# Kernel tuning notes

Measured on AMD Instinct MI355X. Metric: run time of the kernel, lower is better.

Reference implementation:

```python
import jax, jax.numpy as jnp
import numpy as np

EMB = 1280
MD = 200
N = 20000
E = 200000
LN_EPS = 1e-5


def _layer_norm(x, g, b):
    mu = jnp.mean(x, axis=-1, keepdims=True)
    var = jnp.mean((x - mu) ** 2, axis=-1, keepdims=True)
    return (x - mu) * jax.lax.rsqrt(var + LN_EPS) * g + b


def _gat_conv(x, edge_index, edge_attr, W, We, a_src, a_dst, a_edge, bias, heads, C):
    """PyG GATConv (bias-free lin, edge_dim, add_self_loops with fill='mean')."""
    n = x.shape[0]
    src, dst = edge_index[0], edge_index[1]
    # self-loop edge_attr = mean of incoming edge_attr per dst node (0 if none)
    cnt = jax.ops.segment_sum(jnp.ones((edge_attr.shape[0],), x.dtype), dst, n)
    s = jax.ops.segment_sum(edge_attr, dst, n)
    loop_attr = jnp.where(cnt[:, None] > 0, s / jnp.maximum(cnt, 1.0)[:, None], 0.0)
    loop = jnp.arange(n)
    src = jnp.concatenate([src, loop])
    dst = jnp.concatenate([dst, loop])
    ea = jnp.concatenate([edge_attr, loop_attr], axis=0)
    h = (x @ W).reshape(n, heads, C)                      # [N,H,C]
    al_s = jnp.einsum('nhc,hc->nh', h, a_src)
    al_d = jnp.einsum('nhc,hc->nh', h, a_dst)
    eh = (ea @ We).reshape(-1, heads, C)                  # [E+N,H,C]
    al_e = jnp.einsum('ehc,hc->eh', eh, a_edge)
    alpha = jax.nn.leaky_relu(al_s[src] + al_d[dst] + al_e, 0.2)
    amax = jax.ops.segment_max(alpha, dst, n)
    amax = jnp.where(jnp.isfinite(amax), amax, 0.0)
    ex = jnp.exp(alpha - amax[dst])
    denom = jax.ops.segment_sum(ex, dst, n)
    w = ex / (denom[dst] + 1e-16)                         # segment softmax over dst
    out = jax.ops.segment_sum(h[src] * w[:, :, None], dst, n)
    return out.reshape(n, heads * C) + bias


def _forward(x, edge_index, edge_attr,
             ca_qw, ca_qb, ca_kw, ca_kb, ca_vw, ca_vb, ca_ow, ca_ob,
             g0_w, g0_ew, g0_as, g0_ad, g0_ae, g0_b, ln0_g, ln0_b,
             g1_w, g1_ew, g1_as, g1_ad, g1_ae, g1_b, ln1_g, ln1_b,
             g2_w, g2_ew, g2_as, g2_ad, g2_ae, g2_b, ln2_g, ln2_b,
             cls_w1, cls_b1, cls_w2, cls_b2):
    xe = x[:, :EMB]
    md = x[0, EMB:]
    # CrossAttention: single md vector -> K,V are [1,hidden]
    Q = xe @ ca_qw + ca_qb                                # [N,hid]
    K = md @ ca_kw + ca_kb                                # [hid]
    V = md @ ca_vw + ca_vb                                # [hid]
    scores = (Q @ K) / jnp.sqrt(jnp.asarray(Q.shape[-1], Q.dtype))  # [N]
    wts = jax.nn.softmax(scores, axis=0)[:, None]         # softmax over nodes
    attended = wts * V[None, :]                           # [N,hid]
    h = attended @ ca_ow + ca_ob + xe                     # [N,EMB]

    h = _gat_conv(h, edge_index, edge_attr, g0_w, g0_ew, g0_as, g0_ad, g0_ae, g0_b, 4, 256)
    h = jax.nn.relu(_layer_norm(h, ln0_g, ln0_b))
    h = _gat_conv(h, edge_index, edge_attr, g1_w, g1_ew, g1_as, g1_ad, g1_ae, g1_b, 4, 256)
    h = jax.nn.relu(_layer_norm(h, ln1_g, ln1_b))
    h = _gat_conv(h, edge_index, edge_attr, g2_w, g2_ew, g2_as, g2_ad, g2_ae, g2_b, 1, 256)
    h = jax.nn.relu(_layer_norm(h, ln2_g, ln2_b))

    g = jnp.mean(h, axis=0, keepdims=True)                # [1,256]
    g = jax.nn.relu(g @ cls_w1 + cls_b1)
    return g @ cls_w2 + cls_b2                            # [1,2]


def setup_inputs() -> dict:
    key = jax.random.key(0)
    ks = jax.random.split(key, 64)
    i = [0]
    def nrm(shape, scale=0.05):
        i[0] += 1
        return jax.random.normal(ks[i[0]], shape, jnp.float32) * scale
    inp = {}
    inp['x'] = nrm((N, EMB + MD), 1.0)
    inp['edge_index'] = jax.random.randint(ks[60], (2, E), 0, N, jnp.int64 if jax.config.read('jax_enable_x64') else jnp.int32)
    inp['edge_attr'] = jax.random.uniform(ks[61], (E, 1), jnp.float32)
    inp.update(ca_qw=nrm((EMB, 256)), ca_qb=jnp.zeros((256,), jnp.float32),
               ca_kw=nrm((MD, 256)), ca_kb=jnp.zeros((256,), jnp.float32),
               ca_vw=nrm((MD, 256)), ca_vb=jnp.zeros((256,), jnp.float32),
               ca_ow=nrm((256, EMB)), ca_ob=jnp.zeros((EMB,), jnp.float32))
    inp.update(g0_w=nrm((EMB, 1024)), g0_ew=nrm((1, 1024)), g0_as=nrm((4, 256)),
               g0_ad=nrm((4, 256)), g0_ae=nrm((4, 256)), g0_b=jnp.zeros((1024,), jnp.float32),
               ln0_g=jnp.ones((1024,), jnp.float32), ln0_b=jnp.zeros((1024,), jnp.float32))
    inp.update(g1_w=nrm((1024, 1024)), g1_ew=nrm((1, 1024)), g1_as=nrm((4, 256)),
               g1_ad=nrm((4, 256)), g1_ae=nrm((4, 256)), g1_b=jnp.zeros((1024,), jnp.float32),
               ln1_g=jnp.ones((1024,), jnp.float32), ln1_b=jnp.zeros((1024,), jnp.float32))
    inp.update(g2_w=nrm((1024, 256)), g2_ew=nrm((1, 256)), g2_as=nrm((1, 256)),
               g2_ad=nrm((1, 256)), g2_ae=nrm((1, 256)), g2_b=jnp.zeros((256,), jnp.float32),
               ln2_g=jnp.ones((256,), jnp.float32), ln2_b=jnp.zeros((256,), jnp.float32))
    inp.update(cls_w1=nrm((256, 128)), cls_b1=jnp.zeros((128,), jnp.float32),
               cls_w2=nrm((128, 2)), cls_b2=jnp.zeros((2,), jnp.float32))
    return inp


def reference(x, edge_index, edge_attr,
              ca_qw, ca_qb, ca_kw, ca_kb, ca_vw, ca_vb, ca_ow, ca_ob,
              g0_w, g0_ew, g0_as, g0_ad, g0_ae, g0_b, ln0_g, ln0_b,
              g1_w, g1_ew, g1_as, g1_ad, g1_ae, g1_b, ln1_g, ln1_b,
              g2_w, g2_ew, g2_as, g2_ad, g2_ae, g2_b, ln2_g, ln2_b,
              cls_w1, cls_b1, cls_w2, cls_b2):
    return _forward(x, edge_index, edge_attr,
                    ca_qw, ca_qb, ca_kw, ca_kb, ca_vw, ca_vb, ca_ow, ca_ob,
                    g0_w, g0_ew, g0_as, g0_ad, g0_ae, g0_b, ln0_g, ln0_b,
                    g1_w, g1_ew, g1_as, g1_ad, g1_ae, g1_b, ln1_g, ln1_b,
                    g2_w, g2_ew, g2_as, g2_ad, g2_ae, g2_b, ln2_g, ln2_b,
                    cls_w1, cls_b1, cls_w2, cls_b2)
```

## Files before the change

kernel.cpp:

```cpp
#include <hip/hip_runtime.h>
#include <hip/hip_bf16.h>
#include <math.h>

#define N_NODES 20000
#define N_EDGES 200000
#define XROW    1480

typedef __attribute__((ext_vector_type(8))) _Float16 f16x8;
typedef __attribute__((ext_vector_type(8))) unsigned short u16x8;
typedef __attribute__((ext_vector_type(4))) float f32x4v;

__device__ __forceinline__ float wsum(float v){
#pragma unroll
  for (int o=32;o>0;o>>=1) v += __shfl_down(v,o);
  return v;
}
__device__ __forceinline__ float wmax(float v){
#pragma unroll
  for (int o=32;o>0;o>>=1) v = fmaxf(v,__shfl_down(v,o));
  return v;
}
__device__ __forceinline__ float wsum_all(float v){
#pragma unroll
  for (int o=32;o>0;o>>=1) v += __shfl_xor(v,o);
  return v;
}
__device__ __forceinline__ float wmax_all(float v){
#pragma unroll
  for (int o=32;o>0;o>>=1) v = fmaxf(v,__shfl_xor(v,o));
  return v;
}

__device__ __forceinline__ unsigned short f2hu(float f){
  _Float16 h = (_Float16)f;
  return __builtin_bit_cast(unsigned short, h);
}
__device__ __forceinline__ float hu2f(unsigned short u){
  return (float)__builtin_bit_cast(_Float16, u);
}

__device__ __forceinline__ void async_copy16(void* lds, const void* g){
  __builtin_amdgcn_global_load_lds((const __attribute__((address_space(1))) void*)g,
                                   (__attribute__((address_space(3))) void*)lds, 16, 0, 0);
}

__global__ void edge_count_kernel(const int* __restrict__ ei, const float* __restrict__ ea,
                                  int* __restrict__ cnt, float* __restrict__ easum, int E){
  int e = blockIdx.x*256 + threadIdx.x;
  if (e >= E) return;
  int dst = ei[E + e];
  atomicAdd(&cnt[dst], 1);
  atomicAdd(&easum[dst], ea[e]);
}

__launch_bounds__(1024)
__global__ void scan_kernel(const int* __restrict__ cnt, const float* __restrict__ easum,
                            int* __restrict__ off, float* __restrict__ loop_attr, int n){
  __shared__ int buf[1024];
  __shared__ int carry_s;
  if (threadIdx.x==0) carry_s = 0;
  __syncthreads();
  for (int base=0; base<n; base+=1024){
    int i = base + threadIdx.x;
    int v = (i<n)? cnt[i] : 0;
    if (i<n){
      loop_attr[i] = (v>0) ? easum[i]/(float)v : 0.f;
    }
    buf[threadIdx.x] = v;
    __syncthreads();
    for (int d2=1; d2<1024; d2<<=1){
      int tv = (threadIdx.x>=d2)? buf[threadIdx.x-d2] : 0;
      __syncthreads();
      buf[threadIdx.x] += tv;
      __syncthreads();
    }
    if (i<n) off[i] = carry_s + buf[threadIdx.x] - v;
    int tot = buf[1023];
    __syncthreads();
    if (threadIdx.x==0) carry_s += tot;
    __syncthreads();
  }
  if (threadIdx.x==0) off[n] = carry_s;
}

__global__ void edge_fill_kernel(const int* __restrict__ ei, const float* __restrict__ ea,
                                 const int* __restrict__ off, int* __restrict__ fill,
                                 int* __restrict__ csr_src, float* __restrict__ csr_ea, int E){
  int e = blockIdx.x*256 + threadIdx.x;
  if (e >= E) return;
  int dst = ei[E + e];
  int pos = off[dst] + atomicAdd(&fill[dst], 1);
  csr_src[pos] = ei[e];
  csr_ea[pos]  = ea[e];
}

__global__ void x_to_f16(const float* __restrict__ x, unsigned short* __restrict__ xh){
  const int CH4 = 1280/4;
  long total = (long)N_NODES*CH4;
  for (long i = (long)blockIdx.x*256 + threadIdx.x; i < total; i += (long)gridDim.x*256){
    int row = (int)(i / CH4), c4 = (int)(i % CH4);
    float4 v = *(const float4*)(x + (size_t)row*XROW + c4*4);
    ushort4 o;
    o.x = f2hu(v.x); o.y = f2hu(v.y); o.z = f2hu(v.z); o.w = f2hu(v.w);
    *(ushort4*)(xh + (size_t)row*1280 + c4*4) = o;
  }
}

__global__ void wt_f16_kernel(const float* __restrict__ W, int K, int N,
                              unsigned short* __restrict__ Wt){
  __shared__ float tile[32][33];
  int k0 = blockIdx.x*32, n0 = blockIdx.y*32;
  int tx = threadIdx.x & 31, ty = threadIdx.x >> 5;
  for (int r=ty; r<32; r+=8) tile[r][tx] = W[(size_t)(k0+r)*N + n0+tx];
  __syncthreads();
  for (int r=ty; r<32; r+=8){
    float w = tile[tx][r];
    Wt[(size_t)(n0+r)*K + k0+tx] = f2hu(w);
  }
}

__global__ void kv_kernel(const float* __restrict__ x,
                          const float* __restrict__ kw, const float* __restrict__ kb,
                          const float* __restrict__ vw, const float* __restrict__ vb,
                          float* __restrict__ Kv, float* __restrict__ Vv){
  int j = threadIdx.x;
  float ka = kb[j], va = vb[j];
  for (int k=0;k<200;k++){
    float m = x[1280+k];
    ka = fmaf(m, kw[k*256+j], ka);
    va = fmaf(m, vw[k*256+j], va);
  }
  Kv[j]=ka; Vv[j]=va;
}

__global__ void qkvo_kernel(const float* __restrict__ qw, const float* __restrict__ ow,
                            const float* __restrict__ Kv, const float* __restrict__ Vv,
                            float* __restrict__ qK, float* __restrict__ Vo){
  int idx = blockIdx.x*256 + threadIdx.x;
  if (idx < 1280){
    float a=0;
    for (int j=0;j<256;j++) a = fmaf(qw[idx*256+j], Kv[j], a);
    qK[idx]=a;
  } else if (idx < 2560){
    int j = idx-1280;
    float a=0;
    for (int i=0;i<256;i++) a = fmaf(Vv[i], ow[(size_t)i*1280+j], a);
    Vo[j]=a;
  }
}

__global__ void obw_kernel(const float* __restrict__ ob, const float* __restrict__ Vo,
                           const float* __restrict__ W, float* __restrict__ obW, float* __restrict__ VoW){
  int j = blockIdx.x*256 + threadIdx.x;
  float a=0,b=0;
  for (int i=0;i<1280;i++){
    float w = W[(size_t)i*1024+j];
    a = fmaf(ob[i], w, a);
    b = fmaf(Vo[i], w, b);
  }
  obW[j]=a; VoW[j]=b;
}

__launch_bounds__(256)
__global__ void scores_kernel(const float* __restrict__ x, const float* __restrict__ qK,
                              float* __restrict__ scores, int n){
  __shared__ float qs[1280];
  int t = threadIdx.x;
  for (int i=t;i<1280;i+=256) qs[i]=qK[i];
  __syncthreads();
  int wid = t>>6, lane = t&63;
  int node = blockIdx.x*4 + wid;
  if (node >= n) return;
  const float4* row = (const float4*)(x + (size_t)node*XROW);
  float acc = 0;
#pragma unroll
  for (int it=0; it<5; it++){
    float4 v = row[lane + 64*it];
    float4 q = *(const float4*)&qs[4*(lane+64*it)];
    acc += v.x*q.x + v.y*q.y + v.z*q.z + v.w*q.w;
  }
  acc = wsum(acc);
  if (lane==0) scores[node] = acc;
}

__launch_bounds__(1024)
__global__ void softmax_nodes(const float* __restrict__ scores, float* __restrict__ wts, int n){
  __shared__ float red[16];
  int t = threadIdx.x, lane=t&63, wid=t>>6;
  float m = -INFINITY;
  for (int i=t;i<n;i+=1024) m = fmaxf(m, scores[i]);
  m = wmax(m);
  if (lane==0) red[wid]=m;
  __syncthreads();
  if (t==0){ float r=red[0]; for (int k=1;k<16;k++) r=fmaxf(r,red[k]); red[0]=r; }
  __syncthreads();
  float M = red[0];
  __syncthreads();
  float z=0;
  for (int i=t;i<n;i+=1024) z += expf((scores[i]-M)*(1.f/16.f));
  z = wsum(z);
  if (lane==0) red[wid]=z;
  __syncthreads();
  if (t==0){ float r=0; for (int k=0;k<16;k++) r+=red[k]; red[0]=r; }
  __syncthreads();
  float invZ = 1.f/red[0];
  for (int i=t;i<n;i+=1024) wts[i] = expf((scores[i]-M)*(1.f/16.f))*invZ;
}

__launch_bounds__(256)
__global__ void gemm_f16(const unsigned short* __restrict__ A,
                         const unsigned short* __restrict__ B,
                         unsigned short* __restrict__ C, int M, int N, int K,
                         const float* __restrict__ addCol,
                         const float* __restrict__ vCol,
                         const float* __restrict__ wRow,
                         const float* __restrict__ a_src,
                         const float* __restrict__ a_dst,
                         float* __restrict__ als,
                         float* __restrict__ ald,
                         int H)
{
  __shared__ short lds[2*128*64];
  short* As = lds;
  short* Bs = lds + 128*64;

  const int ntc = N >> 7;
  const int sh  = __popc(ntc - 1);
  const int g   = blockIdx.y >> sh;
  const int nt  = blockIdx.y & (ntc - 1);
  const int band = blockIdx.x + (g << 3);
  if (band * 128 >= M) return;

  const int t = threadIdx.x;
  const int w = t>>6, l = t&63;
  const int bm = band*128, bn = nt*128;
  const int wr = (w>>1)*64, wc = (w&1)*64;

  f32x4v acc[4][4];
#pragma unroll
  for (int i=0;i<4;i++)
#pragma unroll
    for (int j=0;j<4;j++) acc[i][j] = (f32x4v){0.f,0.f,0.f,0.f};

  const unsigned short* Ap[4]; const unsigned short* Bp[4];
  int ldsOff[4];
#pragma unroll
  for (int q=0;q<4;q++){
    int p  = (w*4+q)*64 + l;
    int r  = p>>3, pc = p&7;
    int kc = (pc ^ (r&7))*8;
    int rowA = bm + r; if (rowA > M-1) rowA = M-1;
    Ap[q] = A + (size_t)rowA*K + kc;
    Bp[q] = B + (size_t)(bn+r)*K + kc;
    ldsOff[q] = (w*4+q)*64*8;
  }

  for (int k0=0; k0<K; k0+=64){
#pragma unroll
    for (int q=0;q<4;q++) async_copy16(As + ldsOff[q], Ap[q] + k0);
#pragma unroll
    for (int q=0;q<4;q++) async_copy16(Bs + ldsOff[q], Bp[q] + k0);
    __syncthreads();

    const int q4 = l>>4, m16 = l&15;
#pragma unroll
    for (int ks=0; ks<2; ks++){
      f16x8 af[4], bf[4];
      const int c = ks*4 + q4;
#pragma unroll
      for (int i=0;i<4;i++){
        int ra = wr + i*16 + m16;
        af[i] = *(const f16x8*)&As[ra*64 + ((c ^ (ra&7))*8)];
        int rb = wc + i*16 + m16;
        bf[i] = *(const f16x8*)&Bs[rb*64 + ((c ^ (rb&7))*8)];
      }
#pragma unroll
      for (int i=0;i<4;i++)
#pragma unroll
        for (int j=0;j<4;j++)
          acc[i][j] = __builtin_amdgcn_mfma_f32_16x16x32_f16(af[i], bf[j], acc[i][j], 0,0,0);
    }
    __syncthreads();
  }

  const int q4 = l>>4, m16 = l&15;
  const int hd = (bn + wc) >> 8;
  float asv[4], adv[4];
#pragma unroll
  for (int j=0;j<4;j++){
    int n = bn + wc + j*16 + m16;
    asv[j] = a_src[n];
    adv[j] = a_dst[n];
  }
#pragma unroll
  for (int i=0;i<4;i++){
#pragma unroll
    for (int r=0;r<4;r++){
      int m = bm + wr + i*16 + q4*4 + r;
      if (m >= M) continue;
      float wrow = addCol ? wRow[m] : 0.f;
      unsigned short* crow = C + (size_t)m*N;
      float vj[4];
#pragma unroll
      for (int j=0;j<4;j++){
        int n = bn + wc + j*16 + m16;
        float v = acc[i][j][r];
        if (addCol) v += addCol[n] + wrow*vCol[n];
        vj[j] = v;
        crow[n] = f2hu(v);
      }
      float s = vj[0]*asv[0] + vj[1]*asv[1] + vj[2]*asv[2] + vj[3]*asv[3];
      float d = vj[0]*adv[0] + vj[1]*adv[1] + vj[2]*adv[2] + vj[3]*adv[3];
#pragma unroll
      for (int o=1;o<16;o<<=1){ s += __shfl_xor(s,o); d += __shfl_xor(d,o); }
      if (m16 == 0){
        atomicAdd(&als[(size_t)m*H + hd], s);
        atomicAdd(&ald[(size_t)m*H + hd], d);
      }
    }
  }
}

template<int H>
__global__ void we_kernel(const float* __restrict__ We, const float* __restrict__ a_edge,
                          float* __restrict__ we){
  int wid = threadIdx.x>>6, lane = threadIdx.x&63;
  if (wid < H){
    const float4* w4 = (const float4*)(We + wid*256);
    const float4* a4 = (const float4*)(a_edge + wid*256);
    float4 a = w4[lane], b = a4[lane];
    float v = a.x*b.x + a.y*b.y + a.z*b.z + a.w*b.w;
    v = wsum(v);
    if (lane==0) we[wid]=v;
  }
}

template<int H>
__launch_bounds__(256)
__global__ void gat_agg_ln_wave(const unsigned short* __restrict__ hmat,
                           const float* __restrict__ als, const float* __restrict__ ald,
                           const int* __restrict__ off, const int* __restrict__ csr_src,
                           const float* __restrict__ csr_ea, const float* __restrict__ loop_attr,
                           const float* __restrict__ we,
                           const float* __restrict__ bias,
                           const float* __restrict__ ln_g, const float* __restrict__ ln_b,
                           float* __restrict__ outf, unsigned short* __restrict__ outb, int n)
{
  constexpr int OUT = 256*H;
  constexpr int CPL = OUT/64;
  const int wv = threadIdx.x>>6, lane = threadIdx.x&63;
  const int i = blockIdx.x*4 + wv;
  __shared__ float wbuf_s[4][64*H];
  __shared__ int   sbuf_s[4][64];
  if (i >= n) return;
  float* wbuf = wbuf_s[wv];
  int*   sbuf = sbuf_s[wv];

  const int begin = off[i];
  const int deg   = off[i+1]-begin;
  const int S     = deg + 1;

  float aldi[H], wei[H];
#pragma unroll
  for (int hh=0;hh<H;hh++){ aldi[hh]=ald[(size_t)i*H+hh]; wei[hh]=we[hh]; }
  const float lea = loop_attr[i];

  const int head = (lane*CPL) >> 8;
  const int c0   = lane*CPL;
  float acc[CPL];
#pragma unroll
  for (int c=0;c<CPL;c++) acc[c]=0.f;

  if (S <= 64){
    int src = i; float ev = lea;
    if (lane < deg){ src = csr_src[begin+lane]; ev = csr_ea[begin+lane]; }
    const bool act = lane < S;
    float a[H];
#pragma unroll
    for (int hh=0;hh<H;hh++){
      float v = als[(size_t)src*H+hh] + aldi[hh] + ev*wei[hh];
      a[hh] = v>0.f ? v : 0.2f*v;
    }
#pragma unroll
    for (int hh=0;hh<H;hh++){
      float M = wmax_all(act ? a[hh] : -INFINITY);
      float e = act ? __expf(a[hh]-M) : 0.f;
      float Z = wsum_all(e);
      wbuf[lane*H+hh] = e / (Z + 1e-16f);
    }
    sbuf[lane] = src;
    for (int j=0;j<S;j++){
      int sj = sbuf[j];
      float wj = wbuf[j*H+head];
      const unsigned short* row = hmat + (size_t)sj*OUT + c0;
      if constexpr (CPL==16){
        u16x8 r0 = *(const u16x8*)(row);
        u16x8 r1 = *(const u16x8*)(row+8);
#pragma unroll
        for (int c=0;c<8;c++){
          acc[c]   = fmaf(wj, hu2f(r0[c]), acc[c]);
          acc[8+c] = fmaf(wj, hu2f(r1[c]), acc[8+c]);
        }
      } else {
        ushort4 r = *(const ushort4*)(row);
        acc[0]=fmaf(wj,hu2f(r.x),acc[0]); acc[1]=fmaf(wj,hu2f(r.y),acc[1]);
        acc[2]=fmaf(wj,hu2f(r.z),acc[2]); acc[3]=fmaf(wj,hu2f(r.w),acc[3]);
      }
    }
  } else {
    float rm[H];
#pragma unroll
    for (int hh=0;hh<H;hh++) rm[hh] = -INFINITY;
    for (int s=lane; s<S; s+=64){
      int src = (s<deg)? csr_src[begin+s] : i;
      float ev = (s<deg)? csr_ea[begin+s] : lea;
#pragma unroll
      for (int hh=0;hh<H;hh++){
        float v = als[(size_t)src*H+hh] + aldi[hh] + ev*wei[hh];
        v = v>0.f? v : 0.2f*v;
        rm[hh] = fmaxf(rm[hh], v);
      }
    }
    float M[H], es[H];
#pragma unroll
    for (int hh=0;hh<H;hh++){ M[hh]=wmax_all(rm[hh]); es[hh]=0.f; }
    for (int s=lane; s<S; s+=64){
      int src = (s<deg)? csr_src[begin+s] : i;
      float ev = (s<deg)? csr_ea[begin+s] : lea;
#pragma unroll
      for (int hh=0;hh<H;hh++){
        float v = als[(size_t)src*H+hh] + aldi[hh] + ev*wei[hh];
        v = v>0.f? v : 0.2f*v;
        es[hh] += __expf(v - M[hh]);
      }
    }
    float invZ[H];
#pragma unroll
    for (int hh=0;hh<H;hh++) invZ[hh] = 1.f/(wsum_all(es[hh]) + 1e-16f);
    for (int cb=0; cb<S; cb+=64){
      int m = min(64, S-cb);
      int s = cb + lane;
      if (s < S){
        int src = (s<deg)? csr_src[begin+s] : i;
        float ev = (s<deg)? csr_ea[begin+s] : lea;
        sbuf[lane] = src;
#pragma unroll
        for (int hh=0;hh<H;hh++){
          float v = als[(size_t)src*H+hh] + aldi[hh] + ev*wei[hh];
          v = v>0.f? v : 0.2f*v;
          wbuf[lane*H+hh] = __expf(v - M[hh]) * invZ[hh];
        }
      }
      for (int j=0;j<m;j++){
        int sj = sbuf[j];
        float wj = wbuf[j*H+head];
        const unsigned short* row = hmat + (size_t)sj*OUT + c0;
        if constexpr (CPL==16){
          u16x8 r0 = *(const u16x8*)(row);
          u16x8 r1 = *(const u16x8*)(row+8);
#pragma unroll
          for (int c=0;c<8;c++){
            acc[c]   = fmaf(wj, hu2f(r0[c]), acc[c]);
            acc[8+c] = fmaf(wj, hu2f(r1[c]), acc[8+c]);
          }
        } else {
          ushort4 r = *(const ushort4*)(row);
          acc[0]=fmaf(wj,hu2f(r.x),acc[0]); acc[1]=fmaf(wj,hu2f(r.y),acc[1]);
          acc[2]=fmaf(wj,hu2f(r.z),acc[2]); acc[3]=fmaf(wj,hu2f(r.w),acc[3]);
        }
      }
    }
  }

  float vals[CPL];
  float ls=0.f;
#pragma unroll
  for (int c=0;c<CPL;c+=4){
    float4 b4 = *(const float4*)(bias + c0 + c);
    vals[c]=acc[c]+b4.x; vals[c+1]=acc[c+1]+b4.y; vals[c+2]=acc[c+2]+b4.z; vals[c+3]=acc[c+3]+b4.w;
    ls += vals[c]+vals[c+1]+vals[c+2]+vals[c+3];
  }
  float mu = wsum_all(ls) * (1.f/OUT);
  float lv=0.f;
#pragma unroll
  for (int c=0;c<CPL;c++){ float d=vals[c]-mu; lv += d*d; }
  float inv = rsqrtf(wsum_all(lv)*(1.f/OUT) + 1e-5f);

  if (outb){
#pragma unroll
    for (int c=0;c<CPL;c+=8){
      u16x8 o;
#pragma unroll
      for (int k=0;k<8;k++){
        float g = ln_g[c0+c+k], b = ln_b[c0+c+k];
        o[k] = f2hu(fmaxf((vals[c+k]-mu)*inv*g + b, 0.f));
      }
      *(u16x8*)(outb + (size_t)i*OUT + c0 + c) = o;
    }
    if constexpr (CPL==4){
    }
  }
  if (outb && CPL==4){
    ushort4 o;
    o.x = f2hu(fmaxf((vals[0]-mu)*inv*ln_g[c0+0] + ln_b[c0+0], 0.f));
    o.y = f2hu(fmaxf((vals[1]-mu)*inv*ln_g[c0+1] + ln_b[c0+1], 0.f));
    o.z = f2hu(fmaxf((vals[2]-mu)*inv*ln_g[c0+2] + ln_b[c0+2], 0.f));
    o.w = f2hu(fmaxf((vals[3]-mu)*inv*ln_g[c0+3] + ln_b[c0+3], 0.f));
    *(ushort4*)(outb + (size_t)i*OUT + c0) = o;
  }
  if (!outb){
#pragma unroll
    for (int c=0;c<CPL;c+=4){
      float4 g4 = *(const float4*)(ln_g + c0 + c);
      float4 b4 = *(const float4*)(ln_b + c0 + c);
      float4 o;
      o.x = fmaxf((vals[c+0]-mu)*inv*g4.x + b4.x, 0.f);
      o.y = fmaxf((vals[c+1]-mu)*inv*g4.y + b4.y, 0.f);
      o.z = fmaxf((vals[c+2]-mu)*inv*g4.z + b4.z, 0.f);
      o.w = fmaxf((vals[c+3]-mu)*inv*g4.w + b4.w, 0.f);
      *(float4*)(outf + (size_t)i*OUT + c0 + c) = o;
    }
  }
}

__global__ void colsum_kernel(const float* __restrict__ h2, float* __restrict__ gsum, int n){
  int c = threadIdx.x;
  float acc=0;
  for (int i=blockIdx.x;i<n;i+=gridDim.x) acc += h2[(size_t)i*256 + c];
  atomicAdd(&gsum[c], acc);
}

__launch_bounds__(128)
__global__ void cls_kernel(const float* __restrict__ gsum,
                           const float* __restrict__ w1, const float* __restrict__ b1,
                           const float* __restrict__ w2, const float* __restrict__ b2,
                           float* __restrict__ outp){
  __shared__ float g[256];
  __shared__ float hid[128];
  int t = threadIdx.x;
  g[t]     = gsum[t]    *(1.f/N_NODES);
  g[t+128] = gsum[t+128]*(1.f/N_NODES);
  __syncthreads();
  float a = b1[t];
  for (int c=0;c<256;c++) a = fmaf(g[c], w1[c*128+t], a);
  hid[t] = fmaxf(a, 0.f);
  __syncthreads();
  if (t<2){
    float o = b2[t];
    for (int j=0;j<128;j++) o = fmaf(hid[j], w2[j*2+t], o);
    outp[t] = o;
  }
}

extern "C" void kernel_launch(void* const* d_in, const int* in_sizes, int n_in,
                              void* d_out, int out_size, void* d_ws, size_t ws_size,
                              hipStream_t stream)
{
  const float* x      = (const float*)d_in[0];
  const int*   ei     = (const int*)  d_in[1];
  const float* ea     = (const float*)d_in[2];
  const float* ca_qw  = (const float*)d_in[3];
  const float* ca_kw  = (const float*)d_in[5];
  const float* ca_kb  = (const float*)d_in[6];
  const float* ca_vw  = (const float*)d_in[7];
  const float* ca_vb  = (const float*)d_in[8];
  const float* ca_ow  = (const float*)d_in[9];
  const float* ca_ob  = (const float*)d_in[10];
  const float* g0_w   = (const float*)d_in[11];
  const float* g0_ew  = (const float*)d_in[12];
  const float* g0_as  = (const float*)d_in[13];
  const float* g0_ad  = (const float*)d_in[14];
  const float* g0_ae  = (const float*)d_in[15];
  const float* g0_b   = (const float*)d_in[16];
  const float* ln0_g  = (const float*)d_in[17];
  const float* ln0_b  = (const float*)d_in[18];
  const float* g1_w   = (const float*)d_in[19];
  const float* g1_ew  = (const float*)d_in[20];
  const float* g1_as  = (const float*)d_in[21];
  const float* g1_ad  = (const float*)d_in[22];
  const float* g1_ae  = (const float*)d_in[23];
  const float* g1_b   = (const float*)d_in[24];
  const float* ln1_g  = (const float*)d_in[25];
  const float* ln1_b  = (const float*)d_in[26];
  const float* g2_w   = (const float*)d_in[27];
  const float* g2_ew  = (const float*)d_in[28];
  const float* g2_as  = (const float*)d_in[29];
  const float* g2_ad  = (const float*)d_in[30];
  const float* g2_ae  = (const float*)d_in[31];
  const float* g2_b   = (const float*)d_in[32];
  const float* ln2_g  = (const float*)d_in[33];
  const float* ln2_b  = (const float*)d_in[34];
  const float* cls_w1 = (const float*)d_in[35];
  const float* cls_b1 = (const float*)d_in[36];
  const float* cls_w2 = (const float*)d_in[37];
  const float* cls_b2 = (const float*)d_in[38];
  float* outp = (float*)d_out;

  const int N = N_NODES, E = N_EDGES;

  char* base = (char*)d_ws;
  size_t o = 0;
  auto alloc = [&](size_t bytes)->void*{
    void* p = base + o;
    o += (bytes + 255) & ~(size_t)255;
    return p;
  };
  unsigned short* hF   = (unsigned short*)alloc((size_t)N*1024*2);
  unsigned short* Af   = (unsigned short*)alloc((size_t)N*1280*2);
  float*          h2   = (float*)         alloc((size_t)N*256*4);
  unsigned short* Wt   = (unsigned short*)alloc((size_t)1280*1024*2);
  float* als       = (float*)alloc((size_t)2*N*4*4);
  float* ald       = als + (size_t)N*4;
  float* scores    = (float*)alloc((size_t)N*4);
  float* wts       = (float*)alloc((size_t)N*4);
  int*   cnt       = (int*)  alloc((size_t)N*4);
  float* easum     = (float*)alloc((size_t)N*4);
  int*   off       = (int*)  alloc((size_t)(N+1)*4);
  int*   fill      = (int*)  alloc((size_t)N*4);
  int*   csr_src   = (int*)  alloc((size_t)E*4);
  float* csr_ea    = (float*)alloc((size_t)E*4);
  float* loop_attr = (float*)alloc((size_t)N*4);
  float* Kv        = (float*)alloc(256*4);
  float* Vv        = (float*)alloc(256*4);
  float* qK        = (float*)alloc(1280*4);
  float* Vo        = (float*)alloc(1280*4);
  float* obW       = (float*)alloc(1024*4);
  float* VoW       = (float*)alloc(1024*4);
  float* web       = (float*)alloc(16*4);
  float* gsum      = (float*)alloc(256*4);

  hipMemsetAsync(cnt,   0, (size_t)N*4, stream);
  hipMemsetAsync(easum, 0, (size_t)N*4, stream);
  hipMemsetAsync(fill,  0, (size_t)N*4, stream);
  hipMemsetAsync(gsum,  0, 256*4,       stream);

  int eblocks = (E + 255)/256;
  edge_count_kernel<<<eblocks,256,0,stream>>>(ei, ea, cnt, easum, E);
  scan_kernel<<<1,1024,0,stream>>>(cnt, easum, off, loop_attr, N);
  edge_fill_kernel<<<eblocks,256,0,stream>>>(ei, ea, off, fill, csr_src, csr_ea, E);

  x_to_f16<<<2048,256,0,stream>>>(x, Af);

  kv_kernel<<<1,256,0,stream>>>(x, ca_kw, ca_kb, ca_vw, ca_vb, Kv, Vv);
  qkvo_kernel<<<10,256,0,stream>>>(ca_qw, ca_ow, Kv, Vv, qK, Vo);
  obw_kernel<<<4,256,0,stream>>>(ca_ob, Vo, g0_w, obW, VoW);
  scores_kernel<<<(N+3)/4,256,0,stream>>>(x, qK, scores, N);
  softmax_nodes<<<1,1024,0,stream>>>(scores, wts, N);

  const int mTiles  = (N + 127)/128;
  const int mGroups = (mTiles + 7)/8;
  const int NB4 = (N + 3)/4;

  wt_f16_kernel<<<dim3(1280/32, 1024/32),256,0,stream>>>(g0_w, 1280, 1024, Wt);
  hipMemsetAsync(als, 0, (size_t)2*N*4*4, stream);
  gemm_f16<<<dim3(8, mGroups*8),256,0,stream>>>(Af, Wt, hF, N, 1024, 1280, obW, VoW, wts,
                                                g0_as, g0_ad, als, ald, 4);
  we_kernel<4><<<1,256,0,stream>>>(g0_ew, g0_ae, web);
  gat_agg_ln_wave<4><<<NB4,256,0,stream>>>(hF, als, ald, off, csr_src, csr_ea, loop_attr,
                                           web, g0_b, ln0_g, ln0_b, nullptr, Af, N);

  wt_f16_kernel<<<dim3(1024/32, 1024/32),256,0,stream>>>(g1_w, 1024, 1024, Wt);
  hipMemsetAsync(als, 0, (size_t)2*N*4*4, stream);
  gemm_f16<<<dim3(8, mGroups*8),256,0,stream>>>(Af, Wt, hF, N, 1024, 1024, nullptr, nullptr, nullptr,
                                                g1_as, g1_ad, als, ald, 4);
  we_kernel<4><<<1,256,0,stream>>>(g1_ew, g1_ae, web);
  gat_agg_ln_wave<4><<<NB4,256,0,stream>>>(hF, als, ald, off, csr_src, csr_ea, loop_attr,
                                           web, g1_b, ln1_g, ln1_b, nullptr, Af, N);

  wt_f16_kernel<<<dim3(1024/32, 256/32),256,0,stream>>>(g2_w, 1024, 256, Wt);
  hipMemsetAsync(als, 0, (size_t)2*N*4*4, stream);
  gemm_f16<<<dim3(8, mGroups*2),256,0,stream>>>(Af, Wt, hF, N, 256, 1024, nullptr, nullptr, nullptr,
                                                g2_as, g2_ad, als, ald, 1);
  we_kernel<1><<<1,256,0,stream>>>(g2_ew, g2_ae, web);
  gat_agg_ln_wave<1><<<NB4,256,0,stream>>>(hF, als, ald, off, csr_src, csr_ea, loop_attr,
                                           web, g2_b, ln2_g, ln2_b, h2, nullptr, N);

  colsum_kernel<<<256,256,0,stream>>>(h2, gsum, N);
  cls_kernel<<<1,128,0,stream>>>(gsum, cls_w1, cls_b1, cls_w2, cls_b2, outp);

  (void)in_sizes; (void)n_in; (void)out_size; (void)ws_size;
}
```

Measured before the change: 981.5 us.

## Single-pass scan, fp16 scores input, and deterministic partial attention logits

Replaces the looped block scan with a per-thread serial chunk plus a single block scan, removing repeated barrier rounds in the single-block prefix sum. The scores kernel now reads the already converted fp16 copy of x instead of the fp32 rows, halving that read traffic at some precision cost. The GEMM epilogue no longer issues global atomics for the per-head attention logits. It reduces them in LDS, writes per-column-tile partials, and adds a small combine kernel, which also drops the memset before each GEMM.

Result: faster. 901.9 us (-8.1%).

```diff
diff --git a/kernel.cpp b/kernel.cpp
--- a/kernel.cpp
+++ b/kernel.cpp
@@ -57,30 +57,38 @@
 __global__ void scan_kernel(const int* __restrict__ cnt, const float* __restrict__ easum,
                             int* __restrict__ off, float* __restrict__ loop_attr, int n){
   __shared__ int buf[1024];
-  __shared__ int carry_s;
-  if (threadIdx.x==0) carry_s = 0;
-  __syncthreads();
-  for (int base=0; base<n; base+=1024){
-    int i = base + threadIdx.x;
+  const int PER = (N_NODES + 1023)/1024;
+  int t = threadIdx.x;
+  int base = t*PER;
+  int local[PER];
+  int s = 0;
+#pragma unroll
+  for (int k=0;k<PER;k++){
+    int i = base + k;
     int v = (i<n)? cnt[i] : 0;
-    if (i<n){
+    local[k] = v;
+    s += v;
+  }
+  buf[t] = s;
+  __syncthreads();
+  for (int d2=1; d2<1024; d2<<=1){
+    int tv = (t>=d2)? buf[t-d2] : 0;
+    __syncthreads();
+    buf[t] += tv;
+    __syncthreads();
+  }
+  int run = buf[t] - s;
+#pragma unroll
+  for (int k=0;k<PER;k++){
+    int i = base + k;
+    if (i < n){
+      off[i] = run;
+      int v = local[k];
       loop_attr[i] = (v>0) ? easum[i]/(float)v : 0.f;
-    }
-    buf[threadIdx.x] = v;
-    __syncthreads();
-    for (int d2=1; d2<1024; d2<<=1){
-      int tv = (threadIdx.x>=d2)? buf[threadIdx.x-d2] : 0;
-      __syncthreads();
-      buf[threadIdx.x] += tv;
-      __syncthreads();
-    }
-    if (i<n) off[i] = carry_s + buf[threadIdx.x] - v;
-    int tot = buf[1023];
-    __syncthreads();
-    if (threadIdx.x==0) carry_s += tot;
-    __syncthreads();
-  }
-  if (threadIdx.x==0) off[n] = carry_s;
+      run += v;
+    }
+  }
+  if (t == 1023) off[n] = buf[1023];
 }
 
 __global__ void edge_fill_kernel(const int* __restrict__ ei, const float* __restrict__ ea,
@@ -162,7 +170,7 @@
 }
 
 __launch_bounds__(256)
-__global__ void scores_kernel(const float* __restrict__ x, const float* __restrict__ qK,
+__global__ void scores_kernel(const unsigned short* __restrict__ xh, const float* __restrict__ qK,
                               float* __restrict__ scores, int n){
   __shared__ float qs[1280];
   int t = threadIdx.x;
@@ -171,13 +179,16 @@
   int wid = t>>6, lane = t&63;
   int node = blockIdx.x*4 + wid;
   if (node >= n) return;
-  const float4* row = (const float4*)(x + (size_t)node*XROW);
+  const u16x8* row = (const u16x8*)(xh + (size_t)node*1280);
   float acc = 0;
 #pragma unroll
-  for (int it=0; it<5; it++){
-    float4 v = row[lane + 64*it];
-    float4 q = *(const float4*)&qs[4*(lane+64*it)];
-    acc += v.x*q.x + v.y*q.y + v.z*q.z + v.w*q.w;
+  for (int it=0; it<3; it++){
+    int chunk = it*64 + lane;
+    if (chunk < 160){
+      u16x8 v = row[chunk];
+#pragma unroll
+      for (int k=0;k<8;k++) acc = fmaf(hu2f(v[k]), qs[chunk*8+k], acc);
+    }
   }
   acc = wsum(acc);
   if (lane==0) scores[node] = acc;
@@ -216,9 +227,8 @@
                          const float* __restrict__ wRow,
                          const float* __restrict__ a_src,
                          const float* __restrict__ a_dst,
-                         float* __restrict__ als,
-                         float* __restrict__ ald,
-                         int H)
+                         float* __restrict__ alsp,
+                         float* __restrict__ aldp)
 {
   __shared__ short lds[2*128*64];
   short* As = lds;
@@ -235,6 +245,7 @@
   const int w = t>>6, l = t&63;
   const int bm = band*128, bn = nt*128;
   const int wr = (w>>1)*64, wc = (w&1)*64;
+  const int half = w & 1;
 
   f32x4v acc[4][4];
 #pragma unroll
@@ -283,8 +294,9 @@
     __syncthreads();
   }
 
+  float* sred = (float*)lds;
+  float* dred = sred + 256;
   const int q4 = l>>4, m16 = l&15;
-  const int hd = (bn + wc) >> 8;
   float asv[4], adv[4];
 #pragma unroll
   for (int j=0;j<4;j++){
@@ -296,10 +308,9 @@
   for (int i=0;i<4;i++){
 #pragma unroll
     for (int r=0;r<4;r++){
-      int m = bm + wr + i*16 + q4*4 + r;
-      if (m >= M) continue;
-      float wrow = addCol ? wRow[m] : 0.f;
-      unsigned short* crow = C + (size_t)m*N;
+      int rloc = wr + i*16 + q4*4 + r;
+      int m = bm + rloc;
+      float wrow = addCol ? wRow[m < M ? m : M-1] : 0.f;
       float vj[4];
 #pragma unroll
       for (int j=0;j<4;j++){
@@ -307,18 +318,39 @@
         float v = acc[i][j][r];
         if (addCol) v += addCol[n] + wrow*vCol[n];
         vj[j] = v;
-        crow[n] = f2hu(v);
+      }
+      if (m < M){
+        unsigned short* crow = C + (size_t)m*N;
+#pragma unroll
+        for (int j=0;j<4;j++) crow[bn + wc + j*16 + m16] = f2hu(vj[j]);
       }
       float s = vj[0]*asv[0] + vj[1]*asv[1] + vj[2]*asv[2] + vj[3]*asv[3];
       float d = vj[0]*adv[0] + vj[1]*adv[1] + vj[2]*adv[2] + vj[3]*adv[3];
 #pragma unroll
       for (int o=1;o<16;o<<=1){ s += __shfl_xor(s,o); d += __shfl_xor(d,o); }
       if (m16 == 0){
-        atomicAdd(&als[(size_t)m*H + hd], s);
-        atomicAdd(&ald[(size_t)m*H + hd], d);
-      }
-    }
-  }
+        sred[half*128 + rloc] = s;
+        dred[half*128 + rloc] = d;
+      }
+    }
+  }
+  __syncthreads();
+  if (t < 128){
+    int m = bm + t;
+    if (m < M){
+      alsp[(size_t)nt*M + m] = sred[t] + sred[128+t];
+      aldp[(size_t)nt*M + m] = dred[t] + dred[128+t];
+    }
+  }
+}
+
+__global__ void als_combine(const float* __restrict__ alsp, const float* __restrict__ aldp,
+                            float* __restrict__ als, float* __restrict__ ald, int M, int H){
+  int idx = blockIdx.x*256 + threadIdx.x;
+  if (idx >= M*H) return;
+  int m = idx / H, hh = idx - m*H;
+  als[idx] = alsp[(size_t)(2*hh)*M + m] + alsp[(size_t)(2*hh+1)*M + m];
+  ald[idx] = aldp[(size_t)(2*hh)*M + m] + aldp[(size_t)(2*hh+1)*M + m];
 }
 
 template<int H>
@@ -487,28 +519,26 @@
   float inv = rsqrtf(wsum_all(lv)*(1.f/OUT) + 1e-5f);
 
   if (outb){
-#pragma unroll
-    for (int c=0;c<CPL;c+=8){
-      u16x8 o;
-#pragma unroll
-      for (int k=0;k<8;k++){
-        float g = ln_g[c0+c+k], b = ln_b[c0+c+k];
-        o[k] = f2hu(fmaxf((vals[c+k]-mu)*inv*g + b, 0.f));
-      }
-      *(u16x8*)(outb + (size_t)i*OUT + c0 + c) = o;
-    }
-    if constexpr (CPL==4){
-    }
-  }
-  if (outb && CPL==4){
-    ushort4 o;
-    o.x = f2hu(fmaxf((vals[0]-mu)*inv*ln_g[c0+0] + ln_b[c0+0], 0.f));
-    o.y = f2hu(fmaxf((vals[1]-mu)*inv*ln_g[c0+1] + ln_b[c0+1], 0.f));
-    o.z = f2hu(fmaxf((vals[2]-mu)*inv*ln_g[c0+2] + ln_b[c0+2], 0.f));
-    o.w = f2hu(fmaxf((vals[3]-mu)*inv*ln_g[c0+3] + ln_b[c0+3], 0.f));
-    *(ushort4*)(outb + (size_t)i*OUT + c0) = o;
-  }
-  if (!outb){
+    if constexpr (CPL==16){
+#pragma unroll
+      for (int c=0;c<CPL;c+=8){
+        u16x8 o;
+#pragma unroll
+        for (int k=0;k<8;k++){
+          float g = ln_g[c0+c+k], b = ln_b[c0+c+k];
+          o[k] = f2hu(fmaxf((vals[c+k]-mu)*inv*g + b, 0.f));
+        }
+        *(u16x8*)(outb + (size_t)i*OUT + c0 + c) = o;
+      }
+    } else {
+      ushort4 o;
+      o.x = f2hu(fmaxf((vals[0]-mu)*inv*ln_g[c0+0] + ln_b[c0+0], 0.f));
+      o.y = f2hu(fmaxf((vals[1]-mu)*inv*ln_g[c0+1] + ln_b[c0+1], 0.f));
+      o.z = f2hu(fmaxf((vals[2]-mu)*inv*ln_g[c0+2] + ln_b[c0+2], 0.f));
+      o.w = f2hu(fmaxf((vals[3]-mu)*inv*ln_g[c0+3] + ln_b[c0+3], 0.f));
+      *(ushort4*)(outb + (size_t)i*OUT + c0) = o;
+    }
+  } else {
 #pragma unroll
     for (int c=0;c<CPL;c+=4){
       float4 g4 = *(const float4*)(ln_g + c0 + c);
@@ -609,6 +639,8 @@
   unsigned short* Af   = (unsigned short*)alloc((size_t)N*1280*2);
   float*          h2   = (float*)         alloc((size_t)N*256*4);
   unsigned short* Wt   = (unsigned short*)alloc((size_t)1280*1024*2);
+  float* alsp      = (float*)alloc((size_t)8*N*4);
+  float* aldp      = (float*)alloc((size_t)8*N*4);
   float* als       = (float*)alloc((size_t)2*N*4*4);
   float* ald       = als + (size_t)N*4;
   float* scores    = (float*)alloc((size_t)N*4);
@@ -644,7 +676,7 @@
   kv_kernel<<<1,256,0,stream>>>(x, ca_kw, ca_kb, ca_vw, ca_vb, Kv, Vv);
   qkvo_kernel<<<10,256,0,stream>>>(ca_qw, ca_ow, Kv, Vv, qK, Vo);
   obw_kernel<<<4,256,0,stream>>>(ca_ob, Vo, g0_w, obW, VoW);
-  scores_kernel<<<(N+3)/4,256,0,stream>>>(x, qK, scores, N);
+  scores_kernel<<<(N+3)/4,256,0,stream>>>(Af, qK, scores, N);
   softmax_nodes<<<1,1024,0,stream>>>(scores, wts, N);
 
   const int mTiles  = (N + 127)/128;
@@ -652,25 +684,25 @@
   const int NB4 = (N + 3)/4;
 
   wt_f16_kernel<<<dim3(1280/32, 1024/32),256,0,stream>>>(g0_w, 1280, 1024, Wt);
-  hipMemsetAsync(als, 0, (size_t)2*N*4*4, stream);
   gemm_f16<<<dim3(8, mGroups*8),256,0,stream>>>(Af, Wt, hF, N, 1024, 1280, obW, VoW, wts,
-                                                g0_as, g0_ad, als, ald, 4);
+                                                g0_as, g0_ad, alsp, aldp);
+  als_combine<<<(N*4+255)/256,256,0,stream>>>(alsp, aldp, als, ald, N, 4);
   we_kernel<4><<<1,256,0,stream>>>(g0_ew, g0_ae, web);
   gat_agg_ln_wave<4><<<NB4,256,0,stream>>>(hF, als, ald, off, csr_src, csr_ea, loop_attr,
                                            web, g0_b, ln0_g, ln0_b, nullptr, Af, N);
 
   wt_f16_kernel<<<dim3(1024/32, 1024/32),256,0,stream>>>(g1_w, 1024, 1024, Wt);
-  hipMemsetAsync(als, 0, (size_t)2*N*4*4, stream);
   gemm_f16<<<dim3(8, mGroups*8),256,0,stream>>>(Af, Wt, hF, N, 1024, 1024, nullptr, nullptr, nullptr,
-                                                g1_as, g1_ad, als, ald, 4);
+                                                g1_as, g1_ad, alsp, aldp);
+  als_combine<<<(N*4+255)/256,256,0,stream>>>(alsp, aldp, als, ald, N, 4);
   we_kernel<4><<<1,256,0,stream>>>(g1_ew, g1_ae, web);
   gat_agg_ln_wave<4><<<NB4,256,0,stream>>>(hF, als, ald, off, csr_src, csr_ea, loop_attr,
                                            web, g1_b, ln1_g, ln1_b, nullptr, Af, N);
 
   wt_f16_kernel<<<dim3(1024/32, 256/32),256,0,stream>>>(g2_w, 1024, 256, Wt);
-  hipMemsetAsync(als, 0, (size_t)2*N*4*4, stream);
   gemm_f16<<<dim3(8, mGroups*2),256,0,stream>>>(Af, Wt, hF, N, 256, 1024, nullptr, nullptr, nullptr,
-                                                g2_as, g2_ad, als, ald, 1);
+                                                g2_as, g2_ad, alsp, aldp);
+  als_combine<<<(N+255)/256,256,0,stream>>>(alsp, aldp, als, ald, N, 1);
   we_kernel<1><<<1,256,0,stream>>>(g2_ew, g2_ae, web);
   gat_agg_ln_wave<1><<<NB4,256,0,stream>>>(hF, als, ald, off, csr_src, csr_ea, loop_attr,
                                            web, g2_b, ln2_g, ln2_b, h2, nullptr, N);
```
